# Performance work log

Hardware: AMD Instinct MI355X
Metric: run time of the kernel (lower is better)

## Reference

```python
import jax, jax.numpy as jnp
import numpy as np

N_QUBITS = 8
N_PAIRS = 4
PAIRS = [(2 * p, 2 * p + 1) for p in range(N_PAIRS)]
STRENGTH = 0.8
DIM = 2 ** N_QUBITS


def _apply_1q_full(st, G, q):
    # st: (2,)*n complex64 state, G: [2,2] gate on qubit q (qubit 0 = most significant)
    out = jnp.tensordot(G, st, axes=([1], [q]))
    return jnp.moveaxis(out, 0, q)


def _apply_ctrl_full(st, G, c, t):
    # controlled-G: apply G on target axis t only where control axis c == 1
    s0 = jnp.take(st, 0, axis=c)
    s1 = jnp.take(st, 1, axis=c)
    t2 = t if t < c else t - 1
    s1 = jnp.moveaxis(jnp.tensordot(G, s1, axes=([1], [t2])), 0, t2)
    return jnp.stack([s0, s1], axis=c)


def _entangled_base():
    # |0...0> -> H on q1, partial CNOT (controlled-RX(pi*strength)) on (q1,q2) per pair
    st = jnp.zeros((2,) * N_QUBITS, jnp.complex64).at[(0,) * N_QUBITS].set(1.0)
    H = jnp.array([[1.0, 1.0], [1.0, -1.0]], jnp.complex64) / np.float32(np.sqrt(2.0))
    th = np.float32(np.pi * STRENGTH)
    c, s = np.float32(np.cos(th / 2)), np.float32(np.sin(th / 2))
    RX = jnp.array([[c, -1j * s], [-1j * s, c]], jnp.complex64)
    for q1, q2 in PAIRS:
        st = _apply_1q_full(st, H, q1)
        st = _apply_ctrl_full(st, RX, q1, q2)
    return st.reshape(-1)


def _rx(theta):
    # RX(theta) = [[cos t/2, -i sin t/2], [-i sin t/2, cos t/2]], batched over theta shape
    cz = jnp.cos(0.5 * theta).astype(jnp.complex64)
    sz = (-1j) * jnp.sin(0.5 * theta).astype(jnp.complex64)
    return jnp.stack([jnp.stack([cz, sz], -1), jnpp_stack_fix(sz, cz)], -2) if False else jnp.stack([jnp.stack([cz, sz], -1), jnp.stack([sz, cz], -1)], -2)


def _rz(theta):
    ph = (0.5j) * theta.astype(jnp.complex64)
    e0, e1 = jnp.exp(-ph), jnp.exp(ph)
    z = jnp.zeros_like(e0)
    return jnp.stack([jnp.stack([e0, z], -1), jnp.stack([z, e1], -1)], -2)


def _quantum_scores(k_states):
    # k_states: [B,S,2*n_qubits] -> expected pair-agreement score [B,S]
    B, S, _ = k_states.shape
    k = k_states.reshape(B, S, N_QUBITS, 2)
    eye = jnp.eye(2, dtype=jnp.complex64)
    st = jnp.broadcast_to(_entangled_base(), (B, S, DIM))  # fresh entangled register per (b,j)
    for q in range(N_QUBITS):
        th_x, th_z = k[:, :, q, 0], k[:, :, q, 1]
        Gx = jnp.where((th_x > 0)[..., None, None], _rx(th_x), eye)
        Gz = jnp.where((th_z > 0)[..., None, None], _rz(th_z), eye)
        G = jnp.einsum('bsij,bsjk->bsik', Gz, Gx)  # RX applied first, then RZ
        L = 2 ** q
        R = DIM // (2 * L)
        stv = st.reshape(B, S, L, 2, R)
        st = jnp.einsum('bsij,bsljr->bslir', G, stv).reshape(B, S, DIM)
    probs = (st.real ** 2 + st.imag ** 2).reshape((B, S) + (2,) * N_QUBITS)
    score = jnp.zeros((B, S), probs.dtype)
    for q1, q2 in PAIRS:
        axes = tuple(2 + a for a in range(N_QUBITS) if a not in (q1, q2))
        marg = probs.sum(axis=axes)  # [B,S,2,2] joint marginal of the pair
        score = score + marg[..., 0, 0] + marg[..., 1, 1]  # P(measure equal)
    return score / N_PAIRS


def reference(query, key, value, Wq, bq, Wk, bk, Wv, bv, Wo, bo):
    q_states = query @ Wq + bq  # computed as in original forward (unused by scores)
    k_states = key @ Wk + bk    # [B,S,2*n_qubits]
    v_states = value @ Wv + bv  # [B,S,d_model]
    B, S, _ = k_states.shape
    score = _quantum_scores(k_states)  # [B,S]; deterministic expected agreement
    # original loop makes score[b,i,j] independent of i under independent per-(b,i,j) sims
    attn = jnp.broadcast_to(score[:, None, :], (B, S, S))
    w = jax.nn.softmax(attn, axis=-1)
    out = jnp.einsum('bij,bjd->bid', w, v_states)
    return out @ Wo + bo


def setup_inputs() -> dict:
    rng = jax.random.key(0)
    ks = jax.random.split(rng, 8)
    B, S, D = 8, 2048, 512
    nq2 = 2 * N_QUBITS
    f = jax.random.normal
    return {
        'query': f(ks[0], (B, S, D), jnp.float32),
        'key': f(ks[1], (B, S, D), jnp.float32),
        'value': f(ks[2], (B, S, D), jnp.float32),
        'Wq': f(ks[3], (D, nq2), jnp.float32) * 0.05,
        'bq': jnp.zeros((nq2,), jnp.float32),
        'Wk': f(ks[4], (D, nq2), jnp.float32) * 0.05,
        'bk': jnp.zeros((nq2,), jnp.float32),
        'Wv': f(ks[5], (D, D), jnp.float32) * 0.05,
        'bv': jnp.zeros((D,), jnp.float32),
        'Wo': f(ks[6], (D, D), jnp.float32) * 0.05,
        'bo': jnp.zeros((D,), jnp.float32),
    }
```

## Files before the change

### kernel.cpp

```cpp
#include <hip/hip_runtime.h>
#include <math.h>

#define DEV __device__ __forceinline__

struct C2 { float x, y; };
DEV C2 cmul(C2 a, C2 b){ return {a.x*b.x - a.y*b.y, a.x*b.y + a.y*b.x}; }
DEV C2 cadd(C2 a, C2 b){ return {a.x+b.x, a.y+b.y}; }
DEV C2 cscale(C2 a, float s){ return {a.x*s, a.y*s}; }
DEV C2 cnegi(C2 a){ return {a.y, -a.x}; }

__global__ __launch_bounds__(256) void k_scores(const float* __restrict__ key,
                                                const float* __restrict__ Wk,
                                                const float* __restrict__ bk,
                                                float* __restrict__ score)
{
    const int lane = threadIdx.x & 63;
    const int wid  = blockIdx.x * (blockDim.x >> 6) + (threadIdx.x >> 6);
    const int nw   = gridDim.x * (blockDim.x >> 6);

    float4 wk[8][4];
    #pragma unroll
    for (int jj = 0; jj < 4; ++jj) {
        const float4* w0 = (const float4*)(Wk + (4 * lane + jj) * 16);
        const float4* w1 = (const float4*)(Wk + (256 + 4 * lane + jj) * 16);
        #pragma unroll
        for (int q = 0; q < 4; ++q) { wk[jj][q] = w0[q]; wk[4 + jj][q] = w1[q]; }
    }
    const float bkr = bk[lane & 15];
    const float c0 = 0.30901699437494745f;
    const float s0 = 0.9510565162951535f;

    for (int r = wid; r < 16384; r += nw) {
        const float4* kp = (const float4*)(key + (size_t)r * 512);
        float4 k0 = kp[lane];
        float4 k1 = kp[64 + lane];
        float el[8] = {k0.x, k0.y, k0.z, k0.w, k1.x, k1.y, k1.z, k1.w};
        float acc[16];
        #pragma unroll
        for (int k = 0; k < 16; ++k) acc[k] = 0.f;
        #pragma unroll
        for (int j = 0; j < 8; ++j) {
            #pragma unroll
            for (int q = 0; q < 4; ++q) {
                acc[4*q+0] = fmaf(el[j], wk[j][q].x, acc[4*q+0]);
                acc[4*q+1] = fmaf(el[j], wk[j][q].y, acc[4*q+1]);
                acc[4*q+2] = fmaf(el[j], wk[j][q].z, acc[4*q+2]);
                acc[4*q+3] = fmaf(el[j], wk[j][q].w, acc[4*q+3]);
            }
        }
        #pragma unroll
        for (int s = 0; s < 4; ++s) {
            const int m = 1 << s;
            const int bbit = (lane >> s) & 1;
            #pragma unroll
            for (int j = 0; j < (16 >> (s + 1)); ++j) {
                float send = bbit ? acc[2*j] : acc[2*j+1];
                float keep = bbit ? acc[2*j+1] : acc[2*j];
                float got  = __shfl_xor(send, m);
                acc[j] = keep + got;
            }
        }
        float ks = acc[0];
        ks += __shfl_xor(ks, 16);
        ks += __shfl_xor(ks, 32);
        ks += bkr;

        int pp = lane & 3;
        float ax = __shfl(ks, 4*pp+0);
        float az = __shfl(ks, 4*pp+1);
        float bx = __shfl(ks, 4*pp+2);
        float bz = __shfl(ks, 4*pp+3);
        float cxa = 1.f, sxa = 0.f; if (ax > 0.f){ sxa = __sinf(0.5f*ax); cxa = __cosf(0.5f*ax); }
        float cpa = 1.f, spa = 0.f; if (az > 0.f){ spa = __sinf(0.5f*az); cpa = __cosf(0.5f*az); }
        float cxb = 1.f, sxb = 0.f; if (bx > 0.f){ sxb = __sinf(0.5f*bx); cxb = __cosf(0.5f*bx); }
        float cpb = 1.f, spb = 0.f; if (bz > 0.f){ spb = __sinf(0.5f*bz); cpb = __cosf(0.5f*bz); }
        C2 A00{cpa*cxa, -spa*cxa}, A01{-spa*sxa, -cpa*sxa};
        C2 A10{spa*sxa, -cpa*sxa}, A11{ cpa*cxa,  spa*cxa};
        C2 B00{cpb*cxb, -spb*cxb}, B01{-spb*sxb, -cpb*sxb};
        C2 B10{spb*sxb, -cpb*sxb}, B11{ cpb*cxb,  spb*cxb};
        C2 u = cadd(cmul(B00, cadd(A00, cscale(A01, c0))),
                    cscale(cnegi(cmul(A01, B01)), s0));
        C2 v = cadd(cmul(B10, cadd(A10, cscale(A11, c0))),
                    cscale(cnegi(cmul(A11, B11)), s0));
        float ps = u.x*u.x + u.y*u.y + v.x*v.x + v.y*v.y;
        ps += __shfl_xor(ps, 1);
        ps += __shfl_xor(ps, 2);
        if (lane == 0) score[r] = ps * 0.125f;
    }
}

__global__ __launch_bounds__(256) void k_softmax(const float* __restrict__ score,
                                                 float* __restrict__ p)
{
    int b = blockIdx.x, t = threadIdx.x;
    const float* s = score + b * 2048;
    float vals[8]; float m = -1e30f;
    #pragma unroll
    for (int i = 0; i < 8; ++i) { vals[i] = s[t + 256*i]; m = fmaxf(m, vals[i]); }
    __shared__ float red[256];
    red[t] = m; __syncthreads();
    for (int off = 128; off > 0; off >>= 1) {
        if (t < off) red[t] = fmaxf(red[t], red[t + off]);
        __syncthreads();
    }
    m = red[0]; __syncthreads();
    float e[8]; float sum = 0.f;
    #pragma unroll
    for (int i = 0; i < 8; ++i) { e[i] = expf(vals[i] - m); sum += e[i]; }
    red[t] = sum; __syncthreads();
    for (int off = 128; off > 0; off >>= 1) {
        if (t < off) red[t] += red[t + off];
        __syncthreads();
    }
    float inv = 1.f / red[0];
    float* pb = p + b * 2048;
    #pragma unroll
    for (int i = 0; i < 8; ++i) pb[t + 256*i] = e[i] * inv;
}

__global__ __launch_bounds__(256) void k_wsum_partial(const float* __restrict__ value,
                                                      const float* __restrict__ p,
                                                      float* __restrict__ partial)
{
    int c = blockIdx.x;
    int b = blockIdx.y;
    int t = threadIdx.x;
    int col4 = t & 127, rg = t >> 7;
    const float4* vbase = (const float4*)value
        + ((size_t)b*2048 + c*32 + rg*16) * 128 + col4;
    const float* pb = p + b*2048 + c*32 + rg*16;
    float4 acc = {0.f, 0.f, 0.f, 0.f};
    #pragma unroll 4
    for (int j = 0; j < 16; ++j) {
        float w = pb[j];
        float4 v = vbase[(size_t)j * 128];
        acc.x = fmaf(w, v.x, acc.x); acc.y = fmaf(w, v.y, acc.y);
        acc.z = fmaf(w, v.z, acc.z); acc.w = fmaf(w, v.w, acc.w);
    }
    __shared__ float4 tmp[128];
    if (rg) tmp[col4] = acc;
    __syncthreads();
    if (!rg) {
        float4 o = tmp[col4];
        acc.x += o.x; acc.y += o.y; acc.z += o.z; acc.w += o.w;
        ((float4*)partial)[((size_t)b*64 + c) * 128 + col4] = acc;
    }
}

__global__ __launch_bounds__(256) void k_vbar(const float* __restrict__ partial,
                                              float* __restrict__ vbar)
{
    int idx = blockIdx.x * 256 + threadIdx.x;
    int b = idx >> 9, e = idx & 511;
    float s = 0.f;
    #pragma unroll 4
    for (int c = 0; c < 64; ++c) s += partial[((size_t)b*64 + c) * 512 + e];
    vbar[idx] = s;
}

__global__ __launch_bounds__(256) void k_gemm8(const float* __restrict__ xin,
                                               const float* __restrict__ W,
                                               const float* __restrict__ bias,
                                               float* __restrict__ xout)
{
    int dt = blockIdx.x, b = blockIdx.y, t = threadIdx.x;
    int dl = t & 63, q = t >> 6;
    int d = dt * 64 + dl;
    const float* x  = xin + b * 512 + q * 128;
    const float* Wc = W + (size_t)(q * 128) * 512 + d;
    float acc = 0.f;
    #pragma unroll 4
    for (int e = 0; e < 128; ++e) acc = fmaf(x[e], Wc[(size_t)e * 512], acc);
    __shared__ float red[256];
    red[t] = acc; __syncthreads();
    if (t < 64) {
        float tot = red[t] + red[t+64] + red[t+128] + red[t+192] + bias[d];
        xout[b * 512 + d] = tot;
    }
}

__global__ __launch_bounds__(256) void k_broadcast(const float* __restrict__ frow,
                                                   float* __restrict__ out)
{
    const size_t total4 = (size_t)8 * 2048 * 128;
    size_t idx = (size_t)blockIdx.x * blockDim.x + threadIdx.x;
    size_t stride = (size_t)gridDim.x * blockDim.x;
    const float4* f4 = (const float4*)frow;
    float4* o4 = (float4*)out;
    for (size_t i = idx; i < total4; i += stride) {
        size_t b   = i >> 18;
        size_t col = i & 127;
        o4[i] = f4[b * 128 + col];
    }
}

extern "C" void kernel_launch(void* const* d_in, const int* in_sizes, int n_in,
                              void* d_out, int out_size, void* d_ws, size_t ws_size,
                              hipStream_t stream) {
    const float* key   = (const float*)d_in[1];
    const float* value = (const float*)d_in[2];
    const float* Wk    = (const float*)d_in[5];
    const float* bk    = (const float*)d_in[6];
    const float* Wv    = (const float*)d_in[7];
    const float* bv    = (const float*)d_in[8];
    const float* Wo    = (const float*)d_in[9];
    const float* bo    = (const float*)d_in[10];
    float* out = (float*)d_out;
    float* ws  = (float*)d_ws;

    float* score   = ws;
    float* p       = ws + 16384;
    float* partial = ws + 32768;
    float* vbar    = ws + 294912;
    float* ctx     = ws + 299008;
    float* frow    = ws + 303104;

    k_scores      <<<512, 256, 0, stream>>>(key, Wk, bk, score);
    k_softmax     <<<8, 256, 0, stream>>>(score, p);
    k_wsum_partial<<<dim3(64, 8), 256, 0, stream>>>(value, p, partial);
    k_vbar        <<<16, 256, 0, stream>>>(partial, vbar);
    k_gemm8       <<<dim3(8, 8), 256, 0, stream>>>(vbar, Wv, bv, ctx);
    k_gemm8       <<<dim3(8, 8), 256, 0, stream>>>(ctx, Wo, bo, frow);
    k_broadcast   <<<2048, 256, 0, stream>>>(frow, out);
}
```

Before: 193.6 us.

## Fuse softmax normalization into weighted sum and merge gemm with broadcast

Drops the separate softmax kernel by writing unnormalized exp(score) values (no max subtraction, which is safe because scores are bounded in [0,1]) and computing per-chunk weight sums inside the weighted-sum kernel. The vbar reduction and normalization move into the first projection kernel. The output projection kernel now also writes the broadcast output directly, taking seven launches down to four. In exchange, the output GEMM is recomputed by 16 blocks per tile, and a fast exp intrinsic is used.

```diff
diff --git a/kernel.cpp b/kernel.cpp
--- a/kernel.cpp
+++ b/kernel.cpp
@@ -12,7 +12,7 @@
 __global__ __launch_bounds__(256) void k_scores(const float* __restrict__ key,
                                                 const float* __restrict__ Wk,
                                                 const float* __restrict__ bk,
-                                                float* __restrict__ score)
+                                                float* __restrict__ w)
 {
     const int lane = threadIdx.x & 63;
     const int wid  = blockIdx.x * (blockDim.x >> 6) + (threadIdx.x >> 6);
@@ -85,42 +85,14 @@
         float ps = u.x*u.x + u.y*u.y + v.x*v.x + v.y*v.y;
         ps += __shfl_xor(ps, 1);
         ps += __shfl_xor(ps, 2);
-        if (lane == 0) score[r] = ps * 0.125f;
-    }
-}
-
-__global__ __launch_bounds__(256) void k_softmax(const float* __restrict__ score,
-                                                 float* __restrict__ p)
-{
-    int b = blockIdx.x, t = threadIdx.x;
-    const float* s = score + b * 2048;
-    float vals[8]; float m = -1e30f;
-    #pragma unroll
-    for (int i = 0; i < 8; ++i) { vals[i] = s[t + 256*i]; m = fmaxf(m, vals[i]); }
-    __shared__ float red[256];
-    red[t] = m; __syncthreads();
-    for (int off = 128; off > 0; off >>= 1) {
-        if (t < off) red[t] = fmaxf(red[t], red[t + off]);
-        __syncthreads();
-    }
-    m = red[0]; __syncthreads();
-    float e[8]; float sum = 0.f;
-    #pragma unroll
-    for (int i = 0; i < 8; ++i) { e[i] = expf(vals[i] - m); sum += e[i]; }
-    red[t] = sum; __syncthreads();
-    for (int off = 128; off > 0; off >>= 1) {
-        if (t < off) red[t] += red[t + off];
-        __syncthreads();
-    }
-    float inv = 1.f / red[0];
-    float* pb = p + b * 2048;
-    #pragma unroll
-    for (int i = 0; i < 8; ++i) pb[t + 256*i] = e[i] * inv;
-}
-
-__global__ __launch_bounds__(256) void k_wsum_partial(const float* __restrict__ value,
-                                                      const float* __restrict__ p,
-                                                      float* __restrict__ partial)
+        if (lane == 0) w[r] = __expf(ps * 0.125f);
+    }
+}
+
+__global__ __launch_bounds__(256) void k_wsum(const float* __restrict__ value,
+                                              const float* __restrict__ w,
+                                              float* __restrict__ partial,
+                                              float* __restrict__ partialw)
 {
     int c = blockIdx.x;
     int b = blockIdx.y;
@@ -128,14 +100,14 @@
     int col4 = t & 127, rg = t >> 7;
     const float4* vbase = (const float4*)value
         + ((size_t)b*2048 + c*32 + rg*16) * 128 + col4;
-    const float* pb = p + b*2048 + c*32 + rg*16;
+    const float* pb = w + b*2048 + c*32 + rg*16;
     float4 acc = {0.f, 0.f, 0.f, 0.f};
     #pragma unroll 4
     for (int j = 0; j < 16; ++j) {
-        float w = pb[j];
+        float wj = pb[j];
         float4 v = vbase[(size_t)j * 128];
-        acc.x = fmaf(w, v.x, acc.x); acc.y = fmaf(w, v.y, acc.y);
-        acc.z = fmaf(w, v.z, acc.z); acc.w = fmaf(w, v.w, acc.w);
+        acc.x = fmaf(wj, v.x, acc.x); acc.y = fmaf(wj, v.y, acc.y);
+        acc.z = fmaf(wj, v.z, acc.z); acc.w = fmaf(wj, v.w, acc.w);
     }
     __shared__ float4 tmp[128];
     if (rg) tmp[col4] = acc;
@@ -145,53 +117,90 @@
         acc.x += o.x; acc.y += o.y; acc.z += o.z; acc.w += o.w;
         ((float4*)partial)[((size_t)b*64 + c) * 128 + col4] = acc;
     }
-}
-
-__global__ __launch_bounds__(256) void k_vbar(const float* __restrict__ partial,
-                                              float* __restrict__ vbar)
-{
-    int idx = blockIdx.x * 256 + threadIdx.x;
-    int b = idx >> 9, e = idx & 511;
-    float s = 0.f;
-    #pragma unroll 4
-    for (int c = 0; c < 64; ++c) s += partial[((size_t)b*64 + c) * 512 + e];
-    vbar[idx] = s;
-}
-
-__global__ __launch_bounds__(256) void k_gemm8(const float* __restrict__ xin,
-                                               const float* __restrict__ W,
-                                               const float* __restrict__ bias,
-                                               float* __restrict__ xout)
+    if (t < 32) {
+        float wv = w[b*2048 + c*32 + t];
+        wv += __shfl_xor(wv, 1);  wv += __shfl_xor(wv, 2);
+        wv += __shfl_xor(wv, 4);  wv += __shfl_xor(wv, 8);
+        wv += __shfl_xor(wv, 16);
+        if (t == 0) partialw[b*64 + c] = wv;
+    }
+}
+
+__global__ __launch_bounds__(256) void k_ctx(const float* __restrict__ partial,
+                                             const float* __restrict__ partialw,
+                                             const float* __restrict__ Wv,
+                                             const float* __restrict__ bv,
+                                             float* __restrict__ ctx)
 {
     int dt = blockIdx.x, b = blockIdx.y, t = threadIdx.x;
+    __shared__ float vb[512];
+    __shared__ float invS;
+    __shared__ float red[256];
+
+    if (t < 64) {
+        float s = partialw[b * 64 + t];
+        s += __shfl_xor(s, 1);  s += __shfl_xor(s, 2);
+        s += __shfl_xor(s, 4);  s += __shfl_xor(s, 8);
+        s += __shfl_xor(s, 16); s += __shfl_xor(s, 32);
+        if (t == 0) invS = 1.f / s;
+    }
+    float a0 = 0.f, a1 = 0.f;
+    const float* pp = partial + (size_t)b * 64 * 512;
+    #pragma unroll 4
+    for (int c = 0; c < 64; ++c) {
+        a0 += pp[c * 512 + t];
+        a1 += pp[c * 512 + 256 + t];
+    }
+    __syncthreads();
+    vb[t] = a0 * invS; vb[t + 256] = a1 * invS;
+    __syncthreads();
+
     int dl = t & 63, q = t >> 6;
     int d = dt * 64 + dl;
-    const float* x  = xin + b * 512 + q * 128;
-    const float* Wc = W + (size_t)(q * 128) * 512 + d;
+    const float* x  = vb + q * 128;
+    const float* Wc = Wv + (size_t)(q * 128) * 512 + d;
     float acc = 0.f;
     #pragma unroll 4
     for (int e = 0; e < 128; ++e) acc = fmaf(x[e], Wc[(size_t)e * 512], acc);
+    red[t] = acc; __syncthreads();
+    if (t < 64)
+        ctx[b * 512 + dt * 64 + t] = red[t] + red[t+64] + red[t+128] + red[t+192]
+                                   + bv[dt * 64 + t];
+}
+
+__global__ __launch_bounds__(256) void k_out(const float* __restrict__ ctx,
+                                             const float* __restrict__ Wo,
+                                             const float* __restrict__ bo,
+                                             float* __restrict__ out)
+{
+    int dt = blockIdx.x, b = blockIdx.y, is = blockIdx.z, t = threadIdx.x;
+    __shared__ float xs[512];
     __shared__ float red[256];
+    __shared__ float4 frow4[16];
+
+    xs[t]       = ctx[b * 512 + t];
+    xs[t + 256] = ctx[b * 512 + 256 + t];
+    __syncthreads();
+
+    int dl = t & 63, q = t >> 6;
+    int d = dt * 64 + dl;
+    const float* x  = xs + q * 128;
+    const float* Wc = Wo + (size_t)(q * 128) * 512 + d;
+    float acc = 0.f;
+    #pragma unroll 4
+    for (int e = 0; e < 128; ++e) acc = fmaf(x[e], Wc[(size_t)e * 512], acc);
     red[t] = acc; __syncthreads();
-    if (t < 64) {
-        float tot = red[t] + red[t+64] + red[t+128] + red[t+192] + bias[d];
-        xout[b * 512 + d] = tot;
-    }
-}
-
-__global__ __launch_bounds__(256) void k_broadcast(const float* __restrict__ frow,
-                                                   float* __restrict__ out)
-{
-    const size_t total4 = (size_t)8 * 2048 * 128;
-    size_t idx = (size_t)blockIdx.x * blockDim.x + threadIdx.x;
-    size_t stride = (size_t)gridDim.x * blockDim.x;
-    const float4* f4 = (const float4*)frow;
-    float4* o4 = (float4*)out;
-    for (size_t i = idx; i < total4; i += stride) {
-        size_t b   = i >> 18;
-        size_t col = i & 127;
-        o4[i] = f4[b * 128 + col];
-    }
+    if (t < 64)
+        ((float*)frow4)[t] = red[t] + red[t+64] + red[t+128] + red[t+192]
+                           + bo[dt * 64 + t];
+    __syncthreads();
+
+    int col4 = t & 15, r0 = t >> 4;
+    float4 val = frow4[col4];
+    float4* o4 = (float4*)out + ((size_t)b * 2048 + is * 128) * 128 + dt * 16;
+    #pragma unroll
+    for (int rr = r0; rr < 128; rr += 16)
+        o4[(size_t)rr * 128 + col4] = val;
 }
 
 extern "C" void kernel_launch(void* const* d_in, const int* in_sizes, int n_in,
@@ -208,18 +217,13 @@
     float* out = (float*)d_out;
     float* ws  = (float*)d_ws;
 
-    float* score   = ws;
-    float* p       = ws + 16384;
-    float* partial = ws + 32768;
-    float* vbar    = ws + 294912;
-    float* ctx     = ws + 299008;
-    float* frow    = ws + 303104;
-
-    k_scores      <<<512, 256, 0, stream>>>(key, Wk, bk, score);
-    k_softmax     <<<8, 256, 0, stream>>>(score, p);
-    k_wsum_partial<<<dim3(64, 8), 256, 0, stream>>>(value, p, partial);
-    k_vbar        <<<16, 256, 0, stream>>>(partial, vbar);
-    k_gemm8       <<<dim3(8, 8), 256, 0, stream>>>(vbar, Wv, bv, ctx);
-    k_gemm8       <<<dim3(8, 8), 256, 0, stream>>>(ctx, Wo, bo, frow);
-    k_broadcast   <<<2048, 256, 0, stream>>>(frow, out);
-}
+    float* w        = ws;
+    float* partial  = ws + 16384;
+    float* partialw = ws + 278528;
+    float* ctx      = ws + 279040;
+
+    k_scores<<<512, 256, 0, stream>>>(key, Wk, bk, w);
+    k_wsum  <<<dim3(64, 8), 256, 0, stream>>>(value, w, partial, partialw);
+    k_ctx   <<<dim3(8, 8), 256, 0, stream>>>(partial, partialw, Wv, bv, ctx);
+    k_out   <<<dim3(8, 8, 16), 256, 0, stream>>>(ctx, Wo, bo, out);
+}
```

After: 188.9 us. -2.5%, faster.
